# Kernel optimization log

Measured on AMD Instinct MI355X. Metric: run time of the kernel, lower is better.

## Reference

```python
import jax, jax.numpy as jnp
import numpy as np

N_NODES = 50000
N_EDGES = 800000
NFEAT = 512
NHID = 128
NCLASS = 40


def setup_inputs() -> dict:
    key = jax.random.key(0)
    ks = jax.random.split(key, 12)
    s = lambda fan_in: 1.0 / np.sqrt(fan_in)
    return {
        "x": jax.random.normal(ks[0], (N_NODES, NFEAT), dtype=jnp.float32),
        "edge_src": jax.random.randint(ks[1], (N_EDGES,), 0, N_NODES, dtype=jnp.int32),
        "edge_dst": jax.random.randint(ks[2], (N_EDGES,), 0, N_NODES, dtype=jnp.int32),
        "edge_val": jax.random.uniform(ks[3], (N_EDGES,), dtype=jnp.float32) * 0.1,
        # GraphConvolution 1: nfeat -> nhid
        "W1": jax.random.uniform(ks[4], (NFEAT, NHID), jnp.float32, -s(NFEAT), s(NFEAT)),
        "b1": jnp.zeros((NHID,), jnp.float32),
        # res1 Linear: nfeat -> nhid (stored as [in, out])
        "Wr1": jax.random.uniform(ks[5], (NFEAT, NHID), jnp.float32, -s(NFEAT), s(NFEAT)),
        "br1": jnp.zeros((NHID,), jnp.float32),
        # GraphConvolution 2: 2*nhid -> nclass
        "W2": jax.random.uniform(ks[6], (2 * NHID, NCLASS), jnp.float32, -s(2 * NHID), s(2 * NHID)),
        "b2": jnp.zeros((NCLASS,), jnp.float32),
        # res2 Linear: 2*nhid -> nclass
        "Wr2": jax.random.uniform(ks[7], (2 * NHID, NCLASS), jnp.float32, -s(2 * NHID), s(2 * NHID)),
        "br2": jnp.zeros((NCLASS,), jnp.float32),
    }


def _spmm(edge_src, edge_dst, edge_val, support):
    # adj @ support with adj in COO form: out[d] += val * support[s]
    msgs = edge_val[:, None] * support[edge_src]  # [E, F] irregular gather
    return jax.ops.segment_sum(msgs, edge_dst, num_segments=N_NODES)


def reference(x, edge_src, edge_dst, edge_val, W1, b1, Wr1, br1, W2, b2, Wr2, br2):
    # gc1(x, adj) = adj @ (x @ W1) + b1
    gc1 = _spmm(edge_src, edge_dst, edge_val, x @ W1) + b1
    h = jnp.concatenate([jax.nn.relu(gc1), x @ Wr1 + br1], axis=1)  # [N, 2*nhid]
    # dropout is identity in eval mode
    gc2 = _spmm(edge_src, edge_dst, edge_val, h @ W2) + b2
    h2 = gc2 + (h @ Wr2 + br2)
    return jax.nn.log_softmax(h2, axis=1)
```

## Files before the change

kernel.cpp:

```cpp
#include <hip/hip_runtime.h>
#include <stdint.h>

#define N_NODES 50000
#define N_EDGES 800000
#define NFEAT 512
#define NHID 128
#define NCLASS 40
#define NBLK 3125
#define NBUCK 196

typedef __attribute__((ext_vector_type(8))) __bf16 bf16x8;
typedef __attribute__((ext_vector_type(4))) float f32x4;
typedef _Float16 h2 __attribute__((ext_vector_type(2)));

__device__ __forceinline__ uint16_t f2b(float f) {
  uint32_t x = __float_as_uint(f);
  uint32_t r = (x + 0x7fffu + ((x >> 16) & 1u)) >> 16;
  return (uint16_t)r;
}

__global__ void k_cast_x(const float* __restrict__ x, uint16_t* __restrict__ xb) {
  int i = blockIdx.x * 256 + threadIdx.x;
  const float4* p = (const float4*)x + (size_t)i * 2;
  float4 a = p[0], b = p[1];
  union { uint16_t u[8]; uint4 v; } o;
  o.u[0] = f2b(a.x); o.u[1] = f2b(a.y); o.u[2] = f2b(a.z); o.u[3] = f2b(a.w);
  o.u[4] = f2b(b.x); o.u[5] = f2b(b.y); o.u[6] = f2b(b.z); o.u[7] = f2b(b.w);
  ((uint4*)xb)[i] = o.v;
}

__global__ void k_prep(const float* __restrict__ W1, const float* __restrict__ Wr1,
                       const float* __restrict__ W2, const float* __restrict__ Wr2,
                       uint16_t* __restrict__ WT1, uint16_t* __restrict__ WT2) {
  int idx = blockIdx.x * 256 + threadIdx.x;
  if (idx < 131072) {
    int n = idx >> 9, k = idx & 511;
    float v = (n < 128) ? W1[(size_t)k * 128 + n] : Wr1[(size_t)k * 128 + (n - 128)];
    WT1[idx] = f2b(v);
  } else {
    int j = idx - 131072;
    int n = j >> 8, k = j & 255;
    float v = 0.f;
    if (n < 40) v = W2[(size_t)k * 40 + n];
    else if (n < 80) v = Wr2[(size_t)k * 40 + (n - 40)];
    WT2[j] = f2b(v);
  }
}

__global__ void k_p1(const int* __restrict__ dst, int* __restrict__ bc) {
  __shared__ int hist[NBUCK];
  int t = threadIdx.x;
  if (t < NBUCK) hist[t] = 0;
  __syncthreads();
  int d = dst[blockIdx.x * 256 + t];
  atomicAdd(&hist[d >> 8], 1);
  __syncthreads();
  if (t < NBUCK) bc[blockIdx.x * NBUCK + t] = hist[t];
}

__global__ void k_p2(const int* __restrict__ bc, int* __restrict__ bc2,
                     int* __restrict__ bucketTotal) {
  __shared__ int part[256];
  int k = blockIdx.x, t = threadIdx.x;
  int vals[13];
  int s = 0;
  int base = t * 13;
#pragma unroll
  for (int i = 0; i < 13; i++) {
    int idx = base + i;
    int v = (idx < NBLK) ? bc[idx * NBUCK + k] : 0;
    vals[i] = v;
    s += v;
  }
  part[t] = s;
  __syncthreads();
  for (int o = 1; o < 256; o <<= 1) {
    int v = (t >= o) ? part[t - o] : 0;
    __syncthreads();
    part[t] += v;
    __syncthreads();
  }
  int run = (t == 0) ? 0 : part[t - 1];
#pragma unroll
  for (int i = 0; i < 13; i++) {
    int idx = base + i;
    if (idx < NBLK) {
      bc2[k * NBLK + idx] = run;
      run += vals[i];
    }
  }
  if (t == 255) bucketTotal[k] = part[255];
}

__global__ void k_p3(const int* __restrict__ bucketTotal, int* __restrict__ bucketBase) {
  __shared__ int sc[256];
  int t = threadIdx.x;
  sc[t] = (t < NBUCK) ? bucketTotal[t] : 0;
  __syncthreads();
  for (int o = 1; o < 256; o <<= 1) {
    int v = (t >= o) ? sc[t - o] : 0;
    __syncthreads();
    sc[t] += v;
    __syncthreads();
  }
  if (t <= NBUCK) bucketBase[t] = (t == 0) ? 0 : sc[t - 1];
}

__global__ void k_p4(const int* __restrict__ src, const int* __restrict__ dst,
                     const float* __restrict__ val, const int* __restrict__ bc2,
                     const int* __restrict__ bucketBase, int2* __restrict__ esc) {
  __shared__ int start[NBUCK];
  __shared__ int cur[NBUCK];
  int b = blockIdx.x, t = threadIdx.x;
  if (t < NBUCK) {
    start[t] = bucketBase[t] + bc2[t * NBLK + b];
    cur[t] = 0;
  }
  __syncthreads();
  int e = b * 256 + t;
  int d = dst[e];
  int k = d >> 8;
  int r = atomicAdd(&cur[k], 1);
  esc[start[k] + r] = make_int2(src[e] | ((d & 255) << 16), __float_as_int(val[e]));
}

__global__ void k_p5(const int2* __restrict__ esc, const int* __restrict__ bucketBase,
                     int2* __restrict__ es, int* __restrict__ offs) {
  __shared__ int hist[256];
  __shared__ int sc[256];
  __shared__ int cur[256];
  int k = blockIdx.x, t = threadIdx.x;
  int base = bucketBase[k], n = bucketBase[k + 1] - base;
  hist[t] = 0;
  __syncthreads();
  for (int i = t; i < n; i += 256) atomicAdd(&hist[esc[base + i].x >> 16], 1);
  __syncthreads();
  sc[t] = hist[t];
  __syncthreads();
  for (int o = 1; o < 256; o <<= 1) {
    int v = (t >= o) ? sc[t - o] : 0;
    __syncthreads();
    sc[t] += v;
    __syncthreads();
  }
  int excl = (t == 0) ? 0 : sc[t - 1];
  int node = k * 256 + t;
  if (node <= N_NODES) offs[node] = base + excl;
  cur[t] = excl;
  __syncthreads();
  for (int i = t; i < n; i += 256) {
    int2 e = esc[base + i];
    int l = e.x >> 16;
    int r = atomicAdd(&cur[l], 1);
    es[base + r] = make_int2(e.x & 0xFFFF, e.y);
  }
}

__global__ __launch_bounds__(256, 2) void k_gemm1(
    const uint16_t* __restrict__ A, const uint16_t* __restrict__ BT, int M,
    _Float16* __restrict__ S1h, uint16_t* __restrict__ h, const float* __restrict__ br1) {
  __shared__ uint16_t Al[128 * 64];
  __shared__ uint16_t Bl[128 * 64];
  const int tid = threadIdx.x;
  const int w = tid >> 6, lane = tid & 63;
  const int wm = w >> 1, wn = w & 1;
  const int m0 = blockIdx.x * 128;
  const int n0 = blockIdx.y * 128;
  const int K = NFEAT;

  f32x4 acc[4][4];
#pragma unroll
  for (int t = 0; t < 4; t++)
#pragma unroll
    for (int u = 0; u < 4; u++) acc[t][u] = (f32x4)0.f;

  const int lrow = lane >> 3;
  const int lcol = lane & 7;

  for (int kb = 0; kb < K / 64; ++kb) {
    __syncthreads();
    const int k0 = kb * 64;
#pragma unroll
    for (int i = 0; i < 4; i++) {
      int rr = (w * 4 + i) * 8 + lrow;
      int ra = m0 + rr;
      if (ra >= M) ra = M - 1;
      const uint16_t* gA = A + (size_t)ra * K + k0 + lcol * 8;
      __builtin_amdgcn_global_load_lds(
          (const __attribute__((address_space(1))) void*)gA,
          (__attribute__((address_space(3))) void*)&Al[(w * 4 + i) * 512], 16, 0, 0);
      int rb = n0 + rr;
      const uint16_t* gB = BT + (size_t)rb * K + k0 + lcol * 8;
      __builtin_amdgcn_global_load_lds(
          (const __attribute__((address_space(1))) void*)gB,
          (__attribute__((address_space(3))) void*)&Bl[(w * 4 + i) * 512], 16, 0, 0);
    }
    __syncthreads();
#pragma unroll
    for (int s = 0; s < 2; s++) {
      bf16x8 av[4], bv[4];
#pragma unroll
      for (int t = 0; t < 4; t++)
        av[t] = *(const bf16x8*)&Al[(wm * 64 + t * 16 + (lane & 15)) * 64 + s * 32 + (lane >> 4) * 8];
#pragma unroll
      for (int u = 0; u < 4; u++)
        bv[u] = *(const bf16x8*)&Bl[(wn * 64 + u * 16 + (lane & 15)) * 64 + s * 32 + (lane >> 4) * 8];
#pragma unroll
      for (int t = 0; t < 4; t++)
#pragma unroll
        for (int u = 0; u < 4; u++)
          acc[t][u] = __builtin_amdgcn_mfma_f32_16x16x32_bf16(av[t], bv[u], acc[t][u], 0, 0, 0);
    }
  }

  const int cl = lane & 15, rq = lane >> 4;
#pragma unroll
  for (int t = 0; t < 4; t++) {
#pragma unroll
    for (int u = 0; u < 4; u++) {
#pragma unroll
      for (int r = 0; r < 4; r++) {
        int m = m0 + wm * 64 + t * 16 + rq * 4 + r;
        int n = n0 + wn * 64 + u * 16 + cl;
        if (m >= M) continue;
        float v = acc[t][u][r];
        if (n < 128)
          S1h[(size_t)m * 128 + n] = (_Float16)v;
        else
          h[(size_t)m * 256 + n] = f2b(v + br1[n - 128]);
      }
    }
  }
}

__global__ __launch_bounds__(256, 2) void k_gemm2(
    const uint16_t* __restrict__ A, const uint16_t* __restrict__ BT, int M,
    _Float16* __restrict__ S2h, float* __restrict__ oacc,
    const float* __restrict__ b2, const float* __restrict__ br2) {
  __shared__ uint16_t Al[128 * 64];
  __shared__ uint16_t Bl[128 * 64];
  const int tid = threadIdx.x;
  const int w = tid >> 6, lane = tid & 63;
  const int wm = w >> 1, wn = w & 1;
  const int m0 = blockIdx.x * 128;
  const int K = 256;

  f32x4 acc[4][4];
#pragma unroll
  for (int t = 0; t < 4; t++)
#pragma unroll
    for (int u = 0; u < 4; u++) acc[t][u] = (f32x4)0.f;

  const int lrow = lane >> 3;
  const int lcol = lane & 7;

  for (int kb = 0; kb < K / 64; ++kb) {
    __syncthreads();
    const int k0 = kb * 64;
#pragma unroll
    for (int i = 0; i < 4; i++) {
      int rr = (w * 4 + i) * 8 + lrow;
      int ra = m0 + rr;
      if (ra >= M) ra = M - 1;
      const uint16_t* gA = A + (size_t)ra * K + k0 + lcol * 8;
      __builtin_amdgcn_global_load_lds(
          (const __attribute__((address_space(1))) void*)gA,
          (__attribute__((address_space(3))) void*)&Al[(w * 4 + i) * 512], 16, 0, 0);
      const uint16_t* gB = BT + (size_t)rr * K + k0 + lcol * 8;
      __builtin_amdgcn_global_load_lds(
          (const __attribute__((address_space(1))) void*)gB,
          (__attribute__((address_space(3))) void*)&Bl[(w * 4 + i) * 512], 16, 0, 0);
    }
    __syncthreads();
#pragma unroll
    for (int s = 0; s < 2; s++) {
      bf16x8 av[4], bv[4];
#pragma unroll
      for (int t = 0; t < 4; t++)
        av[t] = *(const bf16x8*)&Al[(wm * 64 + t * 16 + (lane & 15)) * 64 + s * 32 + (lane >> 4) * 8];
#pragma unroll
      for (int u = 0; u < 4; u++)
        bv[u] = *(const bf16x8*)&Bl[(wn * 64 + u * 16 + (lane & 15)) * 64 + s * 32 + (lane >> 4) * 8];
#pragma unroll
      for (int t = 0; t < 4; t++)
#pragma unroll
        for (int u = 0; u < 4; u++)
          acc[t][u] = __builtin_amdgcn_mfma_f32_16x16x32_bf16(av[t], bv[u], acc[t][u], 0, 0, 0);
    }
  }

  const int cl = lane & 15, rq = lane >> 4;
#pragma unroll
  for (int t = 0; t < 4; t++) {
#pragma unroll
    for (int u = 0; u < 4; u++) {
#pragma unroll
      for (int r = 0; r < 4; r++) {
        int m = m0 + wm * 64 + t * 16 + rq * 4 + r;
        int n = wn * 64 + u * 16 + cl;
        if (m >= M) continue;
        float v = acc[t][u][r];
        if (n < 40) S2h[(size_t)m * 64 + n] = (_Float16)v;
        else if (n < 64) S2h[(size_t)m * 64 + n] = (_Float16)0.f;
        if (n >= 40 && n < 80) oacc[(size_t)m * 64 + (n - 40)] = v + b2[n - 40] + br2[n - 40];
        else if (n >= 80 && n < 104) oacc[(size_t)m * 64 + (n - 40)] = 0.f;
      }
    }
  }
}

__global__ void k_spmm1_csr(const int* __restrict__ offs, const int2* __restrict__ es,
                            const _Float16* __restrict__ S1h, const float* __restrict__ b1,
                            uint16_t* __restrict__ h) {
  int node = blockIdx.x * 4 + (threadIdx.x >> 6);
  if (node >= N_NODES) return;
  int lane = threadIdx.x & 63;
  int eg = lane >> 4;
  int fg = lane & 15;
  int beg = offs[node], end = offs[node + 1];
  h2 acc[4];
#pragma unroll
  for (int j = 0; j < 4; j++) acc[j] = (h2)(_Float16)0.f;
  for (int p = beg; p < end; p += 4) {
    int pe = p + eg;
    bool ok = pe < end;
    int2 ev = es[ok ? pe : beg];
    float v = ok ? __int_as_float(ev.y) : 0.f;
    _Float16 vh = (_Float16)v;
    h2 vv = {vh, vh};
    uint4 g = *(const uint4*)(S1h + (size_t)ev.x * 128 + fg * 8);
    h2* hp = (h2*)&g;
#pragma unroll
    for (int j = 0; j < 4; j++) acc[j] = vv * hp[j] + acc[j];
  }
#pragma unroll
  for (int j = 0; j < 4; j++) {
    int b16 = __shfl_xor(__builtin_bit_cast(int, acc[j]), 16, 64);
    acc[j] = acc[j] + __builtin_bit_cast(h2, b16);
    int b32 = __shfl_xor(__builtin_bit_cast(int, acc[j]), 32, 64);
    acc[j] = acc[j] + __builtin_bit_cast(h2, b32);
  }
  if (eg == 0) {
    const float4* bp = (const float4*)(b1 + fg * 8);
    float4 ba = bp[0], bb = bp[1];
    float r0 = (float)acc[0][0] + ba.x, r1 = (float)acc[0][1] + ba.y;
    float r2 = (float)acc[1][0] + ba.z, r3 = (float)acc[1][1] + ba.w;
    float r4 = (float)acc[2][0] + bb.x, r5 = (float)acc[2][1] + bb.y;
    float r6 = (float)acc[3][0] + bb.z, r7 = (float)acc[3][1] + bb.w;
    union { uint16_t u[8]; uint4 v; } o;
    o.u[0] = f2b(r0 > 0.f ? r0 : 0.f); o.u[1] = f2b(r1 > 0.f ? r1 : 0.f);
    o.u[2] = f2b(r2 > 0.f ? r2 : 0.f); o.u[3] = f2b(r3 > 0.f ? r3 : 0.f);
    o.u[4] = f2b(r4 > 0.f ? r4 : 0.f); o.u[5] = f2b(r5 > 0.f ? r5 : 0.f);
    o.u[6] = f2b(r6 > 0.f ? r6 : 0.f); o.u[7] = f2b(r7 > 0.f ? r7 : 0.f);
    *(uint4*)(h + (size_t)node * 256 + fg * 8) = o.v;
  }
}

__global__ void k_spmm2_lsm(const int* __restrict__ offs, const int2* __restrict__ es,
                            const _Float16* __restrict__ S2h, const float* __restrict__ oacc,
                            float* __restrict__ out) {
  int node = blockIdx.x * 4 + (threadIdx.x >> 6);
  if (node >= N_NODES) return;
  int lane = threadIdx.x & 63;
  int eg = lane >> 3;
  int fg = lane & 7;
  int beg = offs[node], end = offs[node + 1];
  h2 acc[4];
#pragma unroll
  for (int j = 0; j < 4; j++) acc[j] = (h2)(_Float16)0.f;
  for (int p = beg; p < end; p += 8) {
    int pe = p + eg;
    bool ok = pe < end;
    int2 ev = es[ok ? pe : beg];
    float v = ok ? __int_as_float(ev.y) : 0.f;
    _Float16 vh = (_Float16)v;
    h2 vv = {vh, vh};
    uint4 g = *(const uint4*)(S2h + (size_t)ev.x * 64 + fg * 8);
    h2* hp = (h2*)&g;
#pragma unroll
    for (int j = 0; j < 4; j++) acc[j] = vv * hp[j] + acc[j];
  }
#pragma unroll
  for (int j = 0; j < 4; j++) {
    int b8 = __shfl_xor(__builtin_bit_cast(int, acc[j]), 8, 64);
    acc[j] = acc[j] + __builtin_bit_cast(h2, b8);
    int b16 = __shfl_xor(__builtin_bit_cast(int, acc[j]), 16, 64);
    acc[j] = acc[j] + __builtin_bit_cast(h2, b16);
    int b32 = __shfl_xor(__builtin_bit_cast(int, acc[j]), 32, 64);
    acc[j] = acc[j] + __builtin_bit_cast(h2, b32);
  }
  const float4* op = (const float4*)(oacc + (size_t)node * 64 + fg * 8);
  float4 o0 = op[0], o1 = op[1];
  float v0 = (float)acc[0][0] + o0.x, v1 = (float)acc[0][1] + o0.y;
  float v2 = (float)acc[1][0] + o0.z, v3 = (float)acc[1][1] + o0.w;
  float v4 = (float)acc[2][0] + o1.x, v5 = (float)acc[2][1] + o1.y;
  float v6 = (float)acc[3][0] + o1.z, v7 = (float)acc[3][1] + o1.w;
  bool valid = fg < 5;
  float m01 = v0 > v1 ? v0 : v1, m23 = v2 > v3 ? v2 : v3;
  float m45 = v4 > v5 ? v4 : v5, m67 = v6 > v7 ? v6 : v7;
  float ml = m01 > m23 ? m01 : m23;
  float mh = m45 > m67 ? m45 : m67;
  float mv = ml > mh ? ml : mh;
  mv = valid ? mv : -1e30f;
#pragma unroll
  for (int o = 1; o <= 4; o <<= 1) {
    float t = __shfl_xor(mv, o, 64);
    mv = mv > t ? mv : t;
  }
  float se = 0.f;
  if (valid)
    se = __expf(v0 - mv) + __expf(v1 - mv) + __expf(v2 - mv) + __expf(v3 - mv) +
         __expf(v4 - mv) + __expf(v5 - mv) + __expf(v6 - mv) + __expf(v7 - mv);
#pragma unroll
  for (int o = 1; o <= 4; o <<= 1) se += __shfl_xor(se, o, 64);
  if (eg == 0 && valid) {
    float ls = mv + __logf(se);
    float4 r0 = make_float4(v0 - ls, v1 - ls, v2 - ls, v3 - ls);
    float4 r1 = make_float4(v4 - ls, v5 - ls, v6 - ls, v7 - ls);
    float4* wp = (float4*)(out + (size_t)node * 40 + fg * 8);
    wp[0] = r0;
    wp[1] = r1;
  }
}

extern "C" void kernel_launch(void* const* d_in, const int* in_sizes, int n_in,
                              void* d_out, int out_size, void* d_ws, size_t ws_size,
                              hipStream_t stream) {
  const float* x = (const float*)d_in[0];
  const int* esrc = (const int*)d_in[1];
  const int* edst = (const int*)d_in[2];
  const float* eval = (const float*)d_in[3];
  const float* W1 = (const float*)d_in[4];
  const float* b1 = (const float*)d_in[5];
  const float* Wr1 = (const float*)d_in[6];
  const float* br1 = (const float*)d_in[7];
  const float* W2 = (const float*)d_in[8];
  const float* b2 = (const float*)d_in[9];
  const float* Wr2 = (const float*)d_in[10];
  const float* br2 = (const float*)d_in[11];
  float* out = (float*)d_out;

  char* ws = (char*)d_ws;
  uint16_t* xb   = (uint16_t*)(ws);
  _Float16* S1h  = (_Float16*)(ws + 51200000);
  uint16_t* h    = (uint16_t*)(ws + 64000000);
  uint16_t* WT1  = (uint16_t*)(ws + 89600000);
  uint16_t* WT2  = (uint16_t*)(ws + 89862144);
  _Float16* S2h  = (_Float16*)(ws + 89927680);
  float*    oacc = (float*)(ws + 96327680);
  int*      offs = (int*)(ws + 109127680);
  int2*     es   = (int2*)(ws + 109327696);
  int2*     esc  = (int2*)(ws + 115727696);
  int*      bc   = (int*)(ws + 122127696);
  int*      bc2  = (int*)(ws + 124577696);
  int*      bucketTotal = (int*)(ws + 127027696);
  int*      bucketBase  = (int*)(ws + 127028480);

  k_cast_x<<<12500, 256, 0, stream>>>(x, xb);
  k_prep<<<640, 256, 0, stream>>>(W1, Wr1, W2, Wr2, WT1, WT2);

  k_p1<<<NBLK, 256, 0, stream>>>(edst, bc);
  k_p2<<<NBUCK, 256, 0, stream>>>(bc, bc2, bucketTotal);
  k_p3<<<1, 256, 0, stream>>>(bucketTotal, bucketBase);
  k_p4<<<NBLK, 256, 0, stream>>>(esrc, edst, eval, bc2, bucketBase, esc);
  k_p5<<<NBUCK, 256, 0, stream>>>(esc, bucketBase, es, offs);

  dim3 g1(391, 2);
  k_gemm1<<<g1, 256, 0, stream>>>(xb, WT1, N_NODES, S1h, h, br1);

  k_spmm1_csr<<<(N_NODES + 3) / 4, 256, 0, stream>>>(offs, es, S1h, b1, h);

  k_gemm2<<<391, 256, 0, stream>>>(h, WT2, N_NODES, S2h, oacc, b2, br2);

  k_spmm2_lsm<<<(N_NODES + 3) / 4, 256, 0, stream>>>(offs, es, S2h, oacc, out);
}
```

Before: 334.7 us.

## Fuse preprocessing launches, inline bucket scan, and unroll SpMM edge loops by two

Merges the x cast, weight transpose and dst histogram kernels into one launch, and removes the single-block bucket scan kernel by recomputing the 196-entry scan redundantly inside each p4 and p5 block. The SpMM gather loops for both layers now process two edge batches per iteration so that two independent gathers are in flight per lane. This cuts launch count and serialization between tiny kernels, at the cost of redundant scan work per block and extra registers in the SpMM kernels.

```diff
diff --git a/kernel.cpp b/kernel.cpp
--- a/kernel.cpp
+++ b/kernel.cpp
@@ -19,43 +19,44 @@
   return (uint16_t)r;
 }
 
-__global__ void k_cast_x(const float* __restrict__ x, uint16_t* __restrict__ xb) {
-  int i = blockIdx.x * 256 + threadIdx.x;
-  const float4* p = (const float4*)x + (size_t)i * 2;
-  float4 a = p[0], b = p[1];
-  union { uint16_t u[8]; uint4 v; } o;
-  o.u[0] = f2b(a.x); o.u[1] = f2b(a.y); o.u[2] = f2b(a.z); o.u[3] = f2b(a.w);
-  o.u[4] = f2b(b.x); o.u[5] = f2b(b.y); o.u[6] = f2b(b.z); o.u[7] = f2b(b.w);
-  ((uint4*)xb)[i] = o.v;
-}
-
-__global__ void k_prep(const float* __restrict__ W1, const float* __restrict__ Wr1,
+__global__ void k_pre2(const float* __restrict__ x, uint16_t* __restrict__ xb,
+                       const float* __restrict__ W1, const float* __restrict__ Wr1,
                        const float* __restrict__ W2, const float* __restrict__ Wr2,
-                       uint16_t* __restrict__ WT1, uint16_t* __restrict__ WT2) {
-  int idx = blockIdx.x * 256 + threadIdx.x;
-  if (idx < 131072) {
-    int n = idx >> 9, k = idx & 511;
-    float v = (n < 128) ? W1[(size_t)k * 128 + n] : Wr1[(size_t)k * 128 + (n - 128)];
-    WT1[idx] = f2b(v);
+                       uint16_t* __restrict__ WT1, uint16_t* __restrict__ WT2,
+                       const int* __restrict__ dst, int* __restrict__ bc) {
+  int b = blockIdx.x, t = threadIdx.x;
+  if (b < 12500) {
+    int i = b * 256 + t;
+    const float4* p = (const float4*)x + (size_t)i * 2;
+    float4 a = p[0], c = p[1];
+    union { uint16_t u[8]; uint4 v; } o;
+    o.u[0] = f2b(a.x); o.u[1] = f2b(a.y); o.u[2] = f2b(a.z); o.u[3] = f2b(a.w);
+    o.u[4] = f2b(c.x); o.u[5] = f2b(c.y); o.u[6] = f2b(c.z); o.u[7] = f2b(c.w);
+    ((uint4*)xb)[i] = o.v;
+  } else if (b < 13140) {
+    int idx = (b - 12500) * 256 + t;
+    if (idx < 131072) {
+      int n = idx >> 9, k = idx & 511;
+      float v = (n < 128) ? W1[(size_t)k * 128 + n] : Wr1[(size_t)k * 128 + (n - 128)];
+      WT1[idx] = f2b(v);
+    } else {
+      int j = idx - 131072;
+      int n = j >> 8, k = j & 255;
+      float v = 0.f;
+      if (n < 40) v = W2[(size_t)k * 40 + n];
+      else if (n < 80) v = Wr2[(size_t)k * 40 + (n - 40)];
+      WT2[j] = f2b(v);
+    }
   } else {
-    int j = idx - 131072;
-    int n = j >> 8, k = j & 255;
-    float v = 0.f;
-    if (n < 40) v = W2[(size_t)k * 40 + n];
-    else if (n < 80) v = Wr2[(size_t)k * 40 + (n - 40)];
-    WT2[j] = f2b(v);
-  }
-}
-
-__global__ void k_p1(const int* __restrict__ dst, int* __restrict__ bc) {
-  __shared__ int hist[NBUCK];
-  int t = threadIdx.x;
-  if (t < NBUCK) hist[t] = 0;
-  __syncthreads();
-  int d = dst[blockIdx.x * 256 + t];
-  atomicAdd(&hist[d >> 8], 1);
-  __syncthreads();
-  if (t < NBUCK) bc[blockIdx.x * NBUCK + t] = hist[t];
+    __shared__ int hist[NBUCK];
+    int eb = b - 13140;
+    if (t < NBUCK) hist[t] = 0;
+    __syncthreads();
+    int d = dst[eb * 256 + t];
+    atomicAdd(&hist[d >> 8], 1);
+    __syncthreads();
+    if (t < NBUCK) bc[eb * NBUCK + t] = hist[t];
+  }
 }
 
 __global__ void k_p2(const int* __restrict__ bc, int* __restrict__ bc2,
@@ -92,28 +93,23 @@
   if (t == 255) bucketTotal[k] = part[255];
 }
 
-__global__ void k_p3(const int* __restrict__ bucketTotal, int* __restrict__ bucketBase) {
-  __shared__ int sc[256];
-  int t = threadIdx.x;
-  sc[t] = (t < NBUCK) ? bucketTotal[t] : 0;
-  __syncthreads();
-  for (int o = 1; o < 256; o <<= 1) {
-    int v = (t >= o) ? sc[t - o] : 0;
-    __syncthreads();
-    sc[t] += v;
-    __syncthreads();
-  }
-  if (t <= NBUCK) bucketBase[t] = (t == 0) ? 0 : sc[t - 1];
-}
-
 __global__ void k_p4(const int* __restrict__ src, const int* __restrict__ dst,
                      const float* __restrict__ val, const int* __restrict__ bc2,
-                     const int* __restrict__ bucketBase, int2* __restrict__ esc) {
+                     const int* __restrict__ bucketTotal, int2* __restrict__ esc) {
+  __shared__ int sc[256];
   __shared__ int start[NBUCK];
   __shared__ int cur[NBUCK];
   int b = blockIdx.x, t = threadIdx.x;
+  sc[t] = (t < NBUCK) ? bucketTotal[t] : 0;
+  __syncthreads();
+  for (int o = 1; o < 256; o <<= 1) {
+    int v = (t >= o) ? sc[t - o] : 0;
+    __syncthreads();
+    sc[t] += v;
+    __syncthreads();
+  }
   if (t < NBUCK) {
-    start[t] = bucketBase[t] + bc2[t * NBLK + b];
+    start[t] = ((t == 0) ? 0 : sc[t - 1]) + bc2[t * NBLK + b];
     cur[t] = 0;
   }
   __syncthreads();
@@ -124,13 +120,23 @@
   esc[start[k] + r] = make_int2(src[e] | ((d & 255) << 16), __float_as_int(val[e]));
 }
 
-__global__ void k_p5(const int2* __restrict__ esc, const int* __restrict__ bucketBase,
+__global__ void k_p5(const int2* __restrict__ esc, const int* __restrict__ bucketTotal,
                      int2* __restrict__ es, int* __restrict__ offs) {
+  __shared__ int bsc[256];
   __shared__ int hist[256];
   __shared__ int sc[256];
   __shared__ int cur[256];
   int k = blockIdx.x, t = threadIdx.x;
-  int base = bucketBase[k], n = bucketBase[k + 1] - base;
+  bsc[t] = (t < NBUCK) ? bucketTotal[t] : 0;
+  __syncthreads();
+  for (int o = 1; o < 256; o <<= 1) {
+    int v = (t >= o) ? bsc[t - o] : 0;
+    __syncthreads();
+    bsc[t] += v;
+    __syncthreads();
+  }
+  int base = (k == 0) ? 0 : bsc[k - 1];
+  int n = bsc[k] - base;
   hist[t] = 0;
   __syncthreads();
   for (int i = t; i < n; i += 256) atomicAdd(&hist[esc[base + i].x >> 16], 1);
@@ -321,17 +327,24 @@
   h2 acc[4];
 #pragma unroll
   for (int j = 0; j < 4; j++) acc[j] = (h2)(_Float16)0.f;
-  for (int p = beg; p < end; p += 4) {
-    int pe = p + eg;
-    bool ok = pe < end;
-    int2 ev = es[ok ? pe : beg];
-    float v = ok ? __int_as_float(ev.y) : 0.f;
-    _Float16 vh = (_Float16)v;
-    h2 vv = {vh, vh};
-    uint4 g = *(const uint4*)(S1h + (size_t)ev.x * 128 + fg * 8);
-    h2* hp = (h2*)&g;
-#pragma unroll
-    for (int j = 0; j < 4; j++) acc[j] = vv * hp[j] + acc[j];
+  for (int p = beg; p < end; p += 8) {
+    int pa = p + eg, pb = p + 4 + eg;
+    bool oka = pa < end, okb = pb < end;
+    int2 ea = es[oka ? pa : beg];
+    int2 eb = es[okb ? pb : beg];
+    float va = oka ? __int_as_float(ea.y) : 0.f;
+    float vb = okb ? __int_as_float(eb.y) : 0.f;
+    _Float16 vah = (_Float16)va, vbh = (_Float16)vb;
+    h2 vva = {vah, vah}, vvb = {vbh, vbh};
+    uint4 ga = *(const uint4*)(S1h + (size_t)ea.x * 128 + fg * 8);
+    uint4 gb = *(const uint4*)(S1h + (size_t)eb.x * 128 + fg * 8);
+    h2* ha = (h2*)&ga;
+    h2* hb = (h2*)&gb;
+#pragma unroll
+    for (int j = 0; j < 4; j++) {
+      acc[j] = vva * ha[j] + acc[j];
+      acc[j] = vvb * hb[j] + acc[j];
+    }
   }
 #pragma unroll
   for (int j = 0; j < 4; j++) {
@@ -368,17 +381,24 @@
   h2 acc[4];
 #pragma unroll
   for (int j = 0; j < 4; j++) acc[j] = (h2)(_Float16)0.f;
-  for (int p = beg; p < end; p += 8) {
-    int pe = p + eg;
-    bool ok = pe < end;
-    int2 ev = es[ok ? pe : beg];
-    float v = ok ? __int_as_float(ev.y) : 0.f;
-    _Float16 vh = (_Float16)v;
-    h2 vv = {vh, vh};
-    uint4 g = *(const uint4*)(S2h + (size_t)ev.x * 64 + fg * 8);
-    h2* hp = (h2*)&g;
-#pragma unroll
-    for (int j = 0; j < 4; j++) acc[j] = vv * hp[j] + acc[j];
+  for (int p = beg; p < end; p += 16) {
+    int pa = p + eg, pb = p + 8 + eg;
+    bool oka = pa < end, okb = pb < end;
+    int2 ea = es[oka ? pa : beg];
+    int2 eb = es[okb ? pb : beg];
+    float va = oka ? __int_as_float(ea.y) : 0.f;
+    float vb = okb ? __int_as_float(eb.y) : 0.f;
+    _Float16 vah = (_Float16)va, vbh = (_Float16)vb;
+    h2 vva = {vah, vah}, vvb = {vbh, vbh};
+    uint4 ga = *(const uint4*)(S2h + (size_t)ea.x * 64 + fg * 8);
+    uint4 gb = *(const uint4*)(S2h + (size_t)eb.x * 64 + fg * 8);
+    h2* ha = (h2*)&ga;
+    h2* hb = (h2*)&gb;
+#pragma unroll
+    for (int j = 0; j < 4; j++) {
+      acc[j] = vva * ha[j] + acc[j];
+      acc[j] = vvb * hb[j] + acc[j];
+    }
   }
 #pragma unroll
   for (int j = 0; j < 4; j++) {
@@ -454,16 +474,11 @@
   int*      bc   = (int*)(ws + 122127696);
   int*      bc2  = (int*)(ws + 124577696);
   int*      bucketTotal = (int*)(ws + 127027696);
-  int*      bucketBase  = (int*)(ws + 127028480);
-
-  k_cast_x<<<12500, 256, 0, stream>>>(x, xb);
-  k_prep<<<640, 256, 0, stream>>>(W1, Wr1, W2, Wr2, WT1, WT2);
-
-  k_p1<<<NBLK, 256, 0, stream>>>(edst, bc);
+
+  k_pre2<<<16265, 256, 0, stream>>>(x, xb, W1, Wr1, W2, Wr2, WT1, WT2, edst, bc);
   k_p2<<<NBUCK, 256, 0, stream>>>(bc, bc2, bucketTotal);
-  k_p3<<<1, 256, 0, stream>>>(bucketTotal, bucketBase);
-  k_p4<<<NBLK, 256, 0, stream>>>(esrc, edst, eval, bc2, bucketBase, esc);
-  k_p5<<<NBUCK, 256, 0, stream>>>(esc, bucketBase, es, offs);
+  k_p4<<<NBLK, 256, 0, stream>>>(esrc, edst, eval, bc2, bucketTotal, esc);
+  k_p5<<<NBUCK, 256, 0, stream>>>(esc, bucketTotal, es, offs);
 
   dim3 g1(391, 2);
   k_gemm1<<<g1, 256, 0, stream>>>(xb, WT1, N_NODES, S1h, h, br1);
```

New measurement: 319.9 us. 4.4% less time.
